# Kernel optimization log

Hardware: AMD Instinct MI355X
Metric: run time of the kernel (lower is better)

Reference implementation:

```python
import jax, jax.numpy as jnp
import numpy as np

ALPHA = 0.25
GAMMA = 2.0
EPS = 1e-8


def _lsa(cost):
    """Jonker-Volgenant shortest-augmenting-path linear sum assignment.
    Matches scipy.optimize.linear_sum_assignment for rectangular matrices."""
    cost = np.asarray(cost, dtype=np.float64)
    transposed = cost.shape[0] > cost.shape[1]
    if transposed:
        cost = cost.T
    n, m = cost.shape  # n <= m
    INF = 1e18
    u = np.zeros(n + 1)
    v = np.zeros(m + 1)
    p = np.zeros(m + 1, dtype=np.int64)   # p[j] = row (1-indexed) assigned to col j
    way = np.zeros(m + 1, dtype=np.int64)
    for i in range(1, n + 1):
        p[0] = i
        j0 = 0
        minv = np.full(m + 1, INF)
        used = np.zeros(m + 1, dtype=bool)
        while True:
            used[j0] = True
            i0 = p[j0]
            cur = cost[i0 - 1] - u[i0] - v[1:]
            free = ~used[1:]
            better = free & (cur < minv[1:])
            minv[1:][better] = cur[better]
            way[1:][better] = j0
            masked = np.where(free, minv[1:], INF)
            j1 = int(np.argmin(masked)) + 1
            delta = masked[j1 - 1]
            u[p[used]] += delta
            v[used] -= delta
            minv[1:][free] -= delta
            j0 = j1
            if p[j0] == 0:
                break
        while j0 != 0:  # augment
            j1 = way[j0]
            p[j0] = p[j1]
            j0 = j1
    row_of_col = p[1:] - 1
    cols = np.nonzero(row_of_col >= 0)[0]
    rows = row_of_col[cols]
    if transposed:
        rows, cols = cols, rows
    order = np.argsort(rows)
    return rows[order], cols[order]


def _focal_cost(p):
    """pos_cost - neg_cost for sigmoid probs p, per focal-loss matcher cost."""
    neg = (1.0 - ALPHA) * p ** GAMMA * (-jnp.log(1.0 - p + EPS))
    pos = ALPHA * (1.0 - p) ** GAMMA * (-jnp.log(p + EPS))
    return pos - neg


def _match(rec, loc, targets):
    """rec: [bs, Q, Crec] logits; loc: [bs, Q, Cloc] logits; targets: [bs, nt] int.
    Returns (src_idx, tgt_idx) each [bs, nt] (query index, target index)."""
    nt = targets.shape[1]
    cost_class = jnp.take_along_axis(_focal_cost(jax.nn.sigmoid(rec)),
                                     targets[:, None, :], axis=2)      # [bs, Q, nt]
    cost_pos = _focal_cost(jax.nn.sigmoid(loc))[:, :, :nt]             # tgt_pos = arange(nt)
    C = np.asarray(2.0 * cost_class + cost_pos)                        # [bs, Q, nt]
    src, tgt = [], []
    for b in range(C.shape[0]):  # per-batch Hungarian, as in original
        r, c = _lsa(C[b])
        src.append(r)
        tgt.append(c)
    return jnp.asarray(np.stack(src)), jnp.asarray(np.stack(tgt))


def _ce(logits, labels):
    # F.cross_entropy with mean reduction
    logp = jax.nn.log_softmax(logits, axis=-1)
    return -jnp.mean(jnp.take_along_axis(logp, labels[..., None], axis=-1))


def setup_inputs() -> dict:
    key = jax.random.key(0)
    k1, k2, k3 = jax.random.split(key, 3)
    rec = jax.random.normal(k1, (128, 107, 32, 32), dtype=jnp.float32)
    loc = jax.random.normal(k2, (128, 25, 32, 32), dtype=jnp.float32)
    targets = jax.random.randint(k3, (128, 25), 0, 107, dtype=jnp.int64)
    return {"rec": rec, "loc": loc, "targets": targets}


def reference(rec, loc, targets):
    bs, c_rec, H, W = rec.shape
    c_loc = loc.shape[1]
    nt = targets.shape[1]
    rec = jnp.transpose(rec.reshape(bs, c_rec, H * W), (0, 2, 1))  # [bs, Q, Crec]
    loc = jnp.transpose(loc.reshape(bs, c_loc, H * W), (0, 2, 1))  # [bs, Q, Cloc]
    src_idx, tgt_idx = _match(rec, loc, targets)                   # [bs, nt] each
    rec_m = jnp.take_along_axis(rec, src_idx[:, :, None], axis=1)  # [bs, nt, Crec]
    loc_m = jnp.take_along_axis(loc, src_idx[:, :, None], axis=1)  # [bs, nt, Cloc]
    cls_labels = jnp.take_along_axis(targets, tgt_idx, axis=1)     # [bs, nt]
    pos_labels = tgt_idx                                           # tgt_pos[b, j] == j
    det_rec_losses = _ce(rec_m.reshape(bs * nt, c_rec), cls_labels.reshape(-1))
    pos_losses = _ce(loc_m.reshape(bs * nt, c_loc), pos_labels.reshape(-1))
    return (det_rec_losses, pos_losses)
```

## Files before the change

### kernel.cpp

```cpp
#include <hip/hip_runtime.h>
#include <hip/hip_bf16.h>
#include <math.h>

#define BS   128
#define NT   25
#define CREC 107
#define CLOC 25
#define QN   1024
#define INFD 1e18
#define WSTR 257
__device__ __forceinline__ int widx(int j) {
    int q = j - 1;
    return (q & 3) * WSTR + (q >> 2);
}

__device__ __forceinline__ float focal_cost_f(float x) {
    float p   = 1.0f / (1.0f + __expf(-x));
    float neg = 0.75f * p * p * (-__logf(1.0f - p + 1e-8f));
    float pos = 0.25f * (1.0f - p) * (1.0f - p) * (-__logf(p + 1e-8f));
    return pos - neg;
}

__global__ __launch_bounds__(256)
void rowmin_kernel(const float* __restrict__ rec, const float* __restrict__ loc,
                   const int* __restrict__ targets,
                   float* __restrict__ rowmin_g, int* __restrict__ rowarg_g) {
    const int pid   = blockIdx.x;
    const int b     = pid / NT, r = pid % NT;
    const int tid   = threadIdx.x;
    const int qbase = tid << 2;
    const int tc    = targets[pid];

    float4 r4 = *(const float4*)(rec + ((size_t)b * CREC + tc) * QN + qbase);
    float4 l4 = *(const float4*)(loc + ((size_t)b * CLOC + r)  * QN + qbase);
    float c[4];
    c[0] = 2.0f * focal_cost_f(r4.x) + focal_cost_f(l4.x);
    c[1] = 2.0f * focal_cost_f(r4.y) + focal_cost_f(l4.y);
    c[2] = 2.0f * focal_cost_f(r4.z) + focal_cost_f(l4.z);
    c[3] = 2.0f * focal_cost_f(r4.w) + focal_cost_f(l4.w);

    float bv = c[0]; int bq = qbase;
    #pragma unroll
    for (int m = 1; m < 4; ++m)
        if (c[m] < bv) { bv = c[m]; bq = qbase + m; }
    #pragma unroll
    for (int off = 32; off; off >>= 1) {
        float ov = __shfl_xor(bv, off);
        int   oq = __shfl_xor(bq, off);
        if (ov < bv || (ov == bv && oq < bq)) { bv = ov; bq = oq; }
    }
    __shared__ float bmv[4];
    __shared__ int   bmq[4];
    if ((tid & 63) == 0) { bmv[tid >> 6] = bv; bmq[tid >> 6] = bq; }
    __syncthreads();
    if (tid == 0) {
        float fv = bmv[0]; int fq = bmq[0];
        #pragma unroll
        for (int w = 1; w < 4; ++w) {
            float ov = bmv[w]; int oq = bmq[w];
            if (ov < fv || (ov == fv && oq < fq)) { fv = ov; fq = oq; }
        }
        rowmin_g[pid] = fv; rowarg_g[pid] = fq;
    }
}

__global__ __launch_bounds__(256)
void search_kernel(const float* __restrict__ rec, const float* __restrict__ loc,
                   const int* __restrict__ targets,
                   const float* __restrict__ rowmin_g, const int* __restrict__ rowarg_g,
                   int* __restrict__ pairq_g) {
    const int b     = blockIdx.x;
    const int tid   = threadIdx.x;
    const int wave  = tid >> 6;
    const int lane  = tid & 63;
    const int qbase = tid << 2;

    __shared__ int    way_s[4 * WSTR];
    __shared__ int    p_s[QN + 1];
    __shared__ double u_s[NT + 1];
    __shared__ int    t_s[NT];
    __shared__ float  rowmin_s[NT];
    __shared__ int    rowarg_s[NT];
    __shared__ int    unassigned_s[NT];
    __shared__ int    nun_s;
    __shared__ double candv_s[2][4];
    __shared__ int    candj_s[2][4];

    for (int j = tid; j <= QN; j += 256) p_s[j] = 0;
    if (tid < NT) {
        t_s[tid]      = targets[b * NT + tid];
        rowmin_s[tid] = rowmin_g[b * NT + tid];
        rowarg_s[tid] = rowarg_g[b * NT + tid];
    }
    __syncthreads();

    if (tid == 0) {
        nun_s = 0;
        for (int r = 0; r < NT; ++r) {
            u_s[r + 1] = (double)rowmin_s[r];
            int j = rowarg_s[r] + 1;
            if (p_s[j] == 0) p_s[j] = r + 1;
            else             unassigned_s[nun_s++] = r + 1;
        }
    }
    __syncthreads();
    const int nun = nun_s;

    const size_t rb0 = (size_t)b * CREC * QN;
    const size_t lb0 = (size_t)b * CLOC * QN;

    double v[4] = {0.0, 0.0, 0.0, 0.0};

    for (int s = 0; s < nun; ++s) {
        const int i = unassigned_s[s];
        double minv[4] = {INFD, INFD, INFD, INFD};
        double snap[4] = {0.0, 0.0, 0.0, 0.0};
        double dsum    = 0.0;
        unsigned usedmask = 0;
        int j0 = 0;
        int parity = 0;

        for (;;) {
            int i0;
            if (j0 == 0) {
                i0 = i;
            } else {
                int q0 = j0 - 1;
                if ((q0 >> 2) == tid) {
                    int m = q0 & 3;
                    usedmask |= 1u << m;
                    minv[m] = INFD;
                    snap[m] = dsum;
                }
                i0 = p_s[j0];
            }
            const double ui0 = u_s[i0];
            const float4 r4 = *(const float4*)(rec + rb0 + (size_t)t_s[i0 - 1] * QN + qbase);
            const float4 l4 = *(const float4*)(loc + lb0 + (size_t)(i0 - 1) * QN + qbase);
            float cf[4];
            cf[0] = 2.0f * focal_cost_f(r4.x) + focal_cost_f(l4.x);
            cf[1] = 2.0f * focal_cost_f(r4.y) + focal_cost_f(l4.y);
            cf[2] = 2.0f * focal_cost_f(r4.z) + focal_cost_f(l4.z);
            cf[3] = 2.0f * focal_cost_f(r4.w) + focal_cost_f(l4.w);

            double bestv = INFD; int bestj = QN + 2;
            #pragma unroll
            for (int m = 0; m < 4; ++m) {
                if (!(usedmask & (1u << m))) {
                    const int j = qbase + m + 1;
                    double cur = (double)cf[m] - ui0 - v[m];
                    if (cur < minv[m]) { minv[m] = cur; way_s[widx(j)] = j0; }
                    double mv = minv[m];
                    if (mv < bestv || (mv == bestv && j < bestj)) { bestv = mv; bestj = j; }
                }
            }
            #pragma unroll
            for (int off = 32; off; off >>= 1) {
                double ov = __shfl_xor(bestv, off);
                int    oj = __shfl_xor(bestj, off);
                if (ov < bestv || (ov == bestv && oj < bestj)) { bestv = ov; bestj = oj; }
            }
            if (lane == 0) { candv_s[parity][wave] = bestv; candj_s[parity][wave] = bestj; }
            __syncthreads();
            double delta = candv_s[parity][0]; int j1 = candj_s[parity][0];
            #pragma unroll
            for (int w = 1; w < 4; ++w) {
                double dv = candv_s[parity][w]; int dj = candj_s[parity][w];
                if (dv < delta || (dv == delta && dj < j1)) { delta = dv; j1 = dj; }
            }
            parity ^= 1;
            dsum += delta;

            #pragma unroll
            for (int m = 0; m < 4; ++m) {
                if (usedmask & (1u << m)) v[m]    -= delta;
                else                      minv[m] -= delta;
            }
            j0 = j1;
            if (p_s[j0] == 0) break;
        }

        if (tid == 0) u_s[i] += dsum;
        unsigned mm = usedmask;
        while (mm) {
            int m = __ffs(mm) - 1; mm &= mm - 1;
            u_s[p_s[qbase + m + 1]] += dsum - snap[m];
        }
        __syncthreads();
        if (tid == 0) {
            int jj = j0;
            while (jj != 0) {
                int jn = way_s[widx(jj)];
                p_s[jj] = (jn == 0) ? i : p_s[jn];
                jj = jn;
            }
        }
        __syncthreads();
    }

    for (int j = tid + 1; j <= QN; j += 256)
        if (p_s[j] > 0) pairq_g[b * NT + (p_s[j] - 1)] = j - 1;
}

__global__ __launch_bounds__(64)
void loss_kernel(const float* __restrict__ rec, const float* __restrict__ loc,
                 const int* __restrict__ targets, const int* __restrict__ pairq_g,
                 float* __restrict__ partial) {
    const int pid  = blockIdx.x;
    const int b    = pid / NT, t = pid % NT;
    const int lane = threadIdx.x;
    const int q    = pairq_g[pid];

    const float* rb = rec + (size_t)b * CREC * QN + q;
    float x0 = (lane < CREC)      ? rb[(size_t)lane * QN]        : -1e30f;
    float x1 = (lane + 64 < CREC) ? rb[(size_t)(lane + 64) * QN] : -1e30f;
    float mx = fmaxf(x0, x1);
    #pragma unroll
    for (int off = 32; off; off >>= 1) mx = fmaxf(mx, __shfl_xor(mx, off));
    float e = 0.0f;
    if (lane < CREC)      e += expf(x0 - mx);
    if (lane + 64 < CREC) e += expf(x1 - mx);
    #pragma unroll
    for (int off = 32; off; off >>= 1) e += __shfl_xor(e, off);
    float lse = mx + logf(e);

    const float* lb = loc + (size_t)b * CLOC * QN + q;
    float y = (lane < CLOC) ? lb[(size_t)lane * QN] : -1e30f;
    float my = y;
    #pragma unroll
    for (int off = 32; off; off >>= 1) my = fmaxf(my, __shfl_xor(my, off));
    float ey = (lane < CLOC) ? expf(y - my) : 0.0f;
    #pragma unroll
    for (int off = 32; off; off >>= 1) ey += __shfl_xor(ey, off);
    float lsey = my + logf(ey);

    if (lane == 0) {
        int lab = targets[pid];
        partial[pid]           = lse  - rb[(size_t)lab * QN];
        partial[BS * NT + pid] = lsey - lb[(size_t)t * QN];
    }
}

__global__ __launch_bounds__(256)
void finalize_kernel(const float* __restrict__ partial, float* __restrict__ out) {
    const int tid = threadIdx.x;
    float s0 = 0.0f, s1 = 0.0f;
    for (int i = tid; i < BS * NT; i += 256) {
        s0 += partial[i];
        s1 += partial[BS * NT + i];
    }
    __shared__ float a0[4], a1[4];
    #pragma unroll
    for (int off = 32; off; off >>= 1) { s0 += __shfl_xor(s0, off); s1 += __shfl_xor(s1, off); }
    if ((tid & 63) == 0) { a0[tid >> 6] = s0; a1[tid >> 6] = s1; }
    __syncthreads();
    if (tid == 0) {
        out[0] = (a0[0] + a0[1] + a0[2] + a0[3]) * (1.0f / (BS * NT));
        out[1] = (a1[0] + a1[1] + a1[2] + a1[3]) * (1.0f / (BS * NT));
    }
}

extern "C" void kernel_launch(void* const* d_in, const int* in_sizes, int n_in,
                              void* d_out, int out_size, void* d_ws, size_t ws_size,
                              hipStream_t stream) {
    (void)in_sizes; (void)n_in; (void)out_size; (void)ws_size;
    const float* rec     = (const float*)d_in[0];
    const float* loc     = (const float*)d_in[1];
    const int*   targets = (const int*)d_in[2];
    float* out = (float*)d_out;

    float* rowmin_g = (float*)d_ws;
    int*   rowarg_g = (int*)(rowmin_g + BS * NT);
    int*   pairq_g  = (int*)(rowarg_g + BS * NT);
    float* partial  = (float*)(pairq_g + BS * NT);

    hipLaunchKernelGGL(rowmin_kernel, dim3(BS * NT), dim3(256), 0, stream,
                       rec, loc, targets, rowmin_g, rowarg_g);
    hipLaunchKernelGGL(search_kernel, dim3(BS), dim3(256), 0, stream,
                       rec, loc, targets, rowmin_g, rowarg_g, pairq_g);
    hipLaunchKernelGGL(loss_kernel, dim3(BS * NT), dim3(64), 0, stream,
                       rec, loc, targets, pairq_g, partial);
    hipLaunchKernelGGL(finalize_kernel, dim3(1), dim3(256), 0, stream,
                       partial, out);
}
```

Measured before the change: 155.3 us.

## Precompute cost matrix in rowmin kernel and cheapen search argmin reduction

The rowmin kernel now writes the full per-batch cost matrix (BS*NT*QN floats) to workspace. The serial augmenting-path search reads precomputed costs instead of recomputing sigmoid/log focal costs from rec/loc on every iteration. The wave argmin is also replaced by a float fminf shuffle reduction plus a ballot over matching lanes, so the double-precision shuffles run only for those candidates. This adds a roughly 13MB workspace write and needs the workspace to be large enough.

```diff
diff --git a/kernel.cpp b/kernel.cpp
--- a/kernel.cpp
+++ b/kernel.cpp
@@ -23,7 +23,7 @@
 
 __global__ __launch_bounds__(256)
 void rowmin_kernel(const float* __restrict__ rec, const float* __restrict__ loc,
-                   const int* __restrict__ targets,
+                   const int* __restrict__ targets, float* __restrict__ cost_g,
                    float* __restrict__ rowmin_g, int* __restrict__ rowarg_g) {
     const int pid   = blockIdx.x;
     const int b     = pid / NT, r = pid % NT;
@@ -33,16 +33,17 @@
 
     float4 r4 = *(const float4*)(rec + ((size_t)b * CREC + tc) * QN + qbase);
     float4 l4 = *(const float4*)(loc + ((size_t)b * CLOC + r)  * QN + qbase);
-    float c[4];
-    c[0] = 2.0f * focal_cost_f(r4.x) + focal_cost_f(l4.x);
-    c[1] = 2.0f * focal_cost_f(r4.y) + focal_cost_f(l4.y);
-    c[2] = 2.0f * focal_cost_f(r4.z) + focal_cost_f(l4.z);
-    c[3] = 2.0f * focal_cost_f(r4.w) + focal_cost_f(l4.w);
-
-    float bv = c[0]; int bq = qbase;
-    #pragma unroll
-    for (int m = 1; m < 4; ++m)
-        if (c[m] < bv) { bv = c[m]; bq = qbase + m; }
+    float4 c;
+    c.x = 2.0f * focal_cost_f(r4.x) + focal_cost_f(l4.x);
+    c.y = 2.0f * focal_cost_f(r4.y) + focal_cost_f(l4.y);
+    c.z = 2.0f * focal_cost_f(r4.z) + focal_cost_f(l4.z);
+    c.w = 2.0f * focal_cost_f(r4.w) + focal_cost_f(l4.w);
+    *(float4*)(cost_g + ((size_t)pid << 10) + qbase) = c;
+
+    float bv = c.x; int bq = qbase;
+    if (c.y < bv) { bv = c.y; bq = qbase + 1; }
+    if (c.z < bv) { bv = c.z; bq = qbase + 2; }
+    if (c.w < bv) { bv = c.w; bq = qbase + 3; }
     #pragma unroll
     for (int off = 32; off; off >>= 1) {
         float ov = __shfl_xor(bv, off);
@@ -65,8 +66,7 @@
 }
 
 __global__ __launch_bounds__(256)
-void search_kernel(const float* __restrict__ rec, const float* __restrict__ loc,
-                   const int* __restrict__ targets,
+void search_kernel(const float* __restrict__ cost_g,
                    const float* __restrict__ rowmin_g, const int* __restrict__ rowarg_g,
                    int* __restrict__ pairq_g) {
     const int b     = blockIdx.x;
@@ -78,7 +78,6 @@
     __shared__ int    way_s[4 * WSTR];
     __shared__ int    p_s[QN + 1];
     __shared__ double u_s[NT + 1];
-    __shared__ int    t_s[NT];
     __shared__ float  rowmin_s[NT];
     __shared__ int    rowarg_s[NT];
     __shared__ int    unassigned_s[NT];
@@ -88,7 +87,6 @@
 
     for (int j = tid; j <= QN; j += 256) p_s[j] = 0;
     if (tid < NT) {
-        t_s[tid]      = targets[b * NT + tid];
         rowmin_s[tid] = rowmin_g[b * NT + tid];
         rowarg_s[tid] = rowarg_g[b * NT + tid];
     }
@@ -106,8 +104,7 @@
     __syncthreads();
     const int nun = nun_s;
 
-    const size_t rb0 = (size_t)b * CREC * QN;
-    const size_t lb0 = (size_t)b * CLOC * QN;
+    const float* cb = cost_g + ((size_t)b * NT << 10);
 
     double v[4] = {0.0, 0.0, 0.0, 0.0};
 
@@ -135,13 +132,8 @@
                 i0 = p_s[j0];
             }
             const double ui0 = u_s[i0];
-            const float4 r4 = *(const float4*)(rec + rb0 + (size_t)t_s[i0 - 1] * QN + qbase);
-            const float4 l4 = *(const float4*)(loc + lb0 + (size_t)(i0 - 1) * QN + qbase);
-            float cf[4];
-            cf[0] = 2.0f * focal_cost_f(r4.x) + focal_cost_f(l4.x);
-            cf[1] = 2.0f * focal_cost_f(r4.y) + focal_cost_f(l4.y);
-            cf[2] = 2.0f * focal_cost_f(r4.z) + focal_cost_f(l4.z);
-            cf[3] = 2.0f * focal_cost_f(r4.w) + focal_cost_f(l4.w);
+            const float4 c4 = *(const float4*)(cb + ((size_t)(i0 - 1) << 10) + qbase);
+            const float cf[4] = { c4.x, c4.y, c4.z, c4.w };
 
             double bestv = INFD; int bestj = QN + 2;
             #pragma unroll
@@ -154,13 +146,20 @@
                     if (mv < bestv || (mv == bestv && j < bestj)) { bestv = mv; bestj = j; }
                 }
             }
-            #pragma unroll
-            for (int off = 32; off; off >>= 1) {
-                double ov = __shfl_xor(bestv, off);
-                int    oj = __shfl_xor(bestj, off);
-                if (ov < bestv || (ov == bestv && oj < bestj)) { bestv = ov; bestj = oj; }
-            }
-            if (lane == 0) { candv_s[parity][wave] = bestv; candj_s[parity][wave] = bestj; }
+
+            float own32 = (float)bestv;
+            float w32 = own32;
+            #pragma unroll
+            for (int off = 32; off; off >>= 1) w32 = fminf(w32, __shfl_xor(w32, off));
+            unsigned long long cand = __ballot(own32 == w32);
+            double wv = INFD; int wj = QN + 2;
+            while (cand) {
+                int l = __ffsll(cand) - 1; cand &= cand - 1;
+                double vv = __shfl(bestv, l);
+                int    jj = __shfl(bestj, l);
+                if (vv < wv || (vv == wv && jj < wj)) { wv = vv; wj = jj; }
+            }
+            if (lane == 0) { candv_s[parity][wave] = wv; candj_s[parity][wave] = wj; }
             __syncthreads();
             double delta = candv_s[parity][0]; int j1 = candj_s[parity][0];
             #pragma unroll
@@ -269,15 +268,16 @@
     const int*   targets = (const int*)d_in[2];
     float* out = (float*)d_out;
 
-    float* rowmin_g = (float*)d_ws;
+    float* cost_g   = (float*)d_ws;
+    float* rowmin_g = cost_g + (size_t)BS * NT * QN;
     int*   rowarg_g = (int*)(rowmin_g + BS * NT);
-    int*   pairq_g  = (int*)(rowarg_g + BS * NT);
+    int*   pairq_g  = rowarg_g + BS * NT;
     float* partial  = (float*)(pairq_g + BS * NT);
 
     hipLaunchKernelGGL(rowmin_kernel, dim3(BS * NT), dim3(256), 0, stream,
-                       rec, loc, targets, rowmin_g, rowarg_g);
+                       rec, loc, targets, cost_g, rowmin_g, rowarg_g);
     hipLaunchKernelGGL(search_kernel, dim3(BS), dim3(256), 0, stream,
-                       rec, loc, targets, rowmin_g, rowarg_g, pairq_g);
+                       cost_g, rowmin_g, rowarg_g, pairq_g);
     hipLaunchKernelGGL(loss_kernel, dim3(BS * NT), dim3(64), 0, stream,
                        rec, loc, targets, pairq_g, partial);
     hipLaunchKernelGGL(finalize_kernel, dim3(1), dim3(256), 0, stream,
```

Measured after the change: 141.5 us. 8.9% less time.
